# Performance work log

Hardware: AMD Instinct MI355X
Metric: run time of the kernel (lower is better)

Reference implementation:

```python
import jax, jax.numpy as jnp
import numpy as np

S, D, H, FF = 2048, 1024, 16, 4096
DH = D // H
EPS = 1e-5


def gelu(x):
    return 0.5 * x * (1 + jnp.tanh(jnp.sqrt(2 / jnp.pi) * (x + 0.044715 * jnp.power(x, 3))))


def layer_norm(x, w, b):
    mu = jnp.mean(x, axis=-1, keepdims=True)
    var = jnp.mean(jnp.square(x - mu), axis=-1, keepdims=True)
    return (x - mu) * jnp.power(var + EPS, -0.5) * w + b


def glorot(key, shape):
    fan_in, fan_out = shape[0], shape[1]
    lim = jnp.sqrt(6.0 / (fan_in + fan_out))
    return jax.random.uniform(key, shape, jnp.float32, -lim, lim)


def setup_inputs() -> dict:
    key = jax.random.key(0)
    ks = jax.random.split(key, 6)
    return {
        "x": jax.random.normal(ks[0], (S, D), jnp.float32),
        "W_qkv": glorot(ks[1], (D, 3 * D)),
        "W_o": glorot(ks[2], (D, D)),
        "W1": glorot(ks[3], (D, FF)),
        "b1": jnp.zeros((FF,), jnp.float32),
        "W2": glorot(ks[4], (FF, D)),
        "b2": jnp.zeros((D,), jnp.float32),
        "ln_att_w": jnp.ones((D,), jnp.float32),
        "ln_att_b": jnp.zeros((D,), jnp.float32),
        "ln_mlp_w": jnp.ones((D,), jnp.float32),
        "ln_mlp_b": jnp.zeros((D,), jnp.float32),
    }


def attention(x, W_qkv, W_o):
    qkv = (x @ W_qkv).reshape(S, 3, H, DH)
    q, k, v = qkv[:, 0], qkv[:, 1], qkv[:, 2]  # each [S, H, DH]
    # scores [H, S_q, S_k]
    scores = jnp.einsum("qhd,khd->hqk", q, k) / jnp.sqrt(jnp.float32(DH))
    causal = jnp.tril(jnp.ones((S, S), bool))
    scores = jnp.where(causal[None], scores, -jnp.inf)
    w = jax.nn.softmax(scores, axis=2)
    out = jnp.einsum("hqk,khd->qhd", w, v).reshape(S, D)
    return out @ W_o


def reference(x, W_qkv, W_o, W1, b1, W2, b2, ln_att_w, ln_att_b, ln_mlp_w, ln_mlp_b):
    x = x + attention(layer_norm(x, ln_att_w, ln_att_b), W_qkv, W_o)
    h = layer_norm(x, ln_mlp_w, ln_mlp_b)
    mlp_out = gelu(h @ W1 + b1) @ W2 + b2
    return x + mlp_out
```

## Files before the change

kernel.cpp:

```cpp
#include <hip/hip_runtime.h>
#include <math.h>

typedef __bf16 bf16;
typedef __bf16 bf16x4 __attribute__((ext_vector_type(4)));
typedef __bf16 bf16x8 __attribute__((ext_vector_type(8)));
typedef float f32x4 __attribute__((ext_vector_type(4)));
typedef unsigned short u16;
typedef unsigned short u16x8 __attribute__((ext_vector_type(8)));
typedef unsigned int u32;

__device__ __forceinline__ u16 f2bf(float f) {
  union { float f; u32 u; } v; v.f = f;
  u32 u = v.u;
  return (u16)((u + 0x7FFFu + ((u >> 16) & 1u)) >> 16);
}
__device__ __forceinline__ float bf2f(u16 u) {
  union { u32 u; float f; } v; v.u = (u32)u << 16;
  return v.f;
}

__device__ __forceinline__ f32x4 mfma16(bf16x8 a, bf16x8 b, f32x4 c) {
  return __builtin_amdgcn_mfma_f32_16x16x32_bf16(a, b, c, 0, 0, 0);
}

__device__ __forceinline__ size_t pk_addr(int r, int c, int C) {
  return ((size_t)(r >> 4) * (C >> 5) + (c >> 5)) * 512 +
         ((c >> 3) & 3) * 128 + (r & 15) * 8 + (c & 7);
}

__device__ __forceinline__ void wconv_body(const float* __restrict__ W,
                                           u16* __restrict__ Wt, int K, int N,
                                           int bx, int by) {
  __shared__ float tile[64][65];
  const int k0 = by * 64, n0 = bx * 64;
  const int t = threadIdx.x;
  const int tr = t >> 4;
  const int tc = (t & 15) * 4;
#pragma unroll
  for (int it = 0; it < 4; it++) {
    const int r = tr + it * 16;
    const float4 v = *(const float4*)(W + (size_t)(k0 + r) * N + n0 + tc);
    tile[r][tc] = v.x; tile[r][tc + 1] = v.y; tile[r][tc + 2] = v.z; tile[r][tc + 3] = v.w;
  }
  __syncthreads();
#pragma unroll
  for (int it = 0; it < 4; it++) {
    const int rn = tr + it * 16;
    const int n = n0 + rn;
    const int k = k0 + tc;
    ushort4 o;
    o.x = f2bf(tile[tc][rn]);
    o.y = f2bf(tile[tc + 1][rn]);
    o.z = f2bf(tile[tc + 2][rn]);
    o.w = f2bf(tile[tc + 3][rn]);
    *(ushort4*)(Wt + pk_addr(n, k, K)) = o;
  }
}

__global__ __launch_bounds__(256)
void wconv_all(const float* __restrict__ Wqkv, const float* __restrict__ Wo,
               const float* __restrict__ W1, const float* __restrict__ W2,
               u16* __restrict__ Wqkv_t, u16* __restrict__ Wo_t,
               u16* __restrict__ W1_t, u16* __restrict__ W2_t) {
  const int id = blockIdx.x;
  if (id < 768)       { wconv_body(Wqkv, Wqkv_t, 1024, 3072, id % 48, id / 48); }
  else if (id < 1024) { const int j = id - 768;  wconv_body(Wo, Wo_t, 1024, 1024, j % 16, j / 16); }
  else if (id < 2048) { const int j = id - 1024; wconv_body(W1, W1_t, 1024, 4096, j % 64, j / 64); }
  else                { const int j = id - 2048; wconv_body(W2, W2_t, 4096, 1024, j % 16, j / 16); }
}

__global__ __launch_bounds__(256)
void ln_bf16(const float* __restrict__ x, const float* __restrict__ w,
             const float* __restrict__ b, u16* __restrict__ out) {
  const int row = blockIdx.x;
  const int t = threadIdx.x;
  const float4 v = *(const float4*)(x + (size_t)row * 1024 + t * 4);
  float s = v.x + v.y + v.z + v.w;
  float s2 = v.x * v.x + v.y * v.y + v.z * v.z + v.w * v.w;
#pragma unroll
  for (int m = 1; m < 64; m <<= 1) {
    s += __shfl_xor(s, m);
    s2 += __shfl_xor(s2, m);
  }
  __shared__ float red[8];
  if ((t & 63) == 0) { red[t >> 6] = s; red[4 + (t >> 6)] = s2; }
  __syncthreads();
  s = red[0] + red[1] + red[2] + red[3];
  s2 = red[4] + red[5] + red[6] + red[7];
  const float mu = s * (1.f / 1024.f);
  const float var = fmaxf(s2 * (1.f / 1024.f) - mu * mu, 0.f);
  const float rstd = rsqrtf(var + 1e-5f);
  const float* wp = w + t * 4;
  const float* bp = b + t * 4;
  ushort4 o;
  o.x = f2bf((v.x - mu) * rstd * wp[0] + bp[0]);
  o.y = f2bf((v.y - mu) * rstd * wp[1] + bp[1]);
  o.z = f2bf((v.z - mu) * rstd * wp[2] + bp[2]);
  o.w = f2bf((v.w - mu) * rstd * wp[3] + bp[3]);
  *(ushort4*)(out + pk_addr(row, t * 4, 1024)) = o;
}

__global__ __launch_bounds__(256)
void reduce_ln(const float* __restrict__ x, const u16* __restrict__ pb,
               const float* __restrict__ w, const float* __restrict__ b,
               float* __restrict__ x2, u16* __restrict__ h2) {
  const int row = blockIdx.x;
  const int t = threadIdx.x;
  const size_t base = (size_t)row * 1024 + t * 4;
  float4 v = *(const float4*)(x + base);
#pragma unroll
  for (int z = 0; z < 4; z++) {
    const ushort4 p = *(const ushort4*)(pb + (size_t)z * 2097152 + base);
    v.x += bf2f(p.x); v.y += bf2f(p.y); v.z += bf2f(p.z); v.w += bf2f(p.w);
  }
  *(float4*)(x2 + base) = v;
  float s = v.x + v.y + v.z + v.w;
  float s2 = v.x * v.x + v.y * v.y + v.z * v.z + v.w * v.w;
#pragma unroll
  for (int m = 1; m < 64; m <<= 1) {
    s += __shfl_xor(s, m);
    s2 += __shfl_xor(s2, m);
  }
  __shared__ float red[8];
  if ((t & 63) == 0) { red[t >> 6] = s; red[4 + (t >> 6)] = s2; }
  __syncthreads();
  s = red[0] + red[1] + red[2] + red[3];
  s2 = red[4] + red[5] + red[6] + red[7];
  const float mu = s * (1.f / 1024.f);
  const float var = fmaxf(s2 * (1.f / 1024.f) - mu * mu, 0.f);
  const float rstd = rsqrtf(var + 1e-5f);
  const float* wp = w + t * 4;
  const float* bp = b + t * 4;
  ushort4 o;
  o.x = f2bf((v.x - mu) * rstd * wp[0] + bp[0]);
  o.y = f2bf((v.y - mu) * rstd * wp[1] + bp[1]);
  o.z = f2bf((v.z - mu) * rstd * wp[2] + bp[2]);
  o.w = f2bf((v.w - mu) * rstd * wp[3] + bp[3]);
  *(ushort4*)(h2 + pk_addr(row, t * 4, 1024)) = o;
}

__global__ __launch_bounds__(256)
void reduce_out(const float* __restrict__ x2, const float* __restrict__ bias,
                const u16* __restrict__ pb, float* __restrict__ out) {
  const size_t base = ((size_t)blockIdx.x * 256 + threadIdx.x) * 4;
  const int col = (int)(base & 1023);
  float4 v = *(const float4*)(x2 + base);
  const float4 bb = *(const float4*)(bias + col);
  v.x += bb.x; v.y += bb.y; v.z += bb.z; v.w += bb.w;
#pragma unroll
  for (int z = 0; z < 4; z++) {
    const ushort4 p = *(const ushort4*)(pb + (size_t)z * 2097152 + base);
    v.x += bf2f(p.x); v.y += bf2f(p.y); v.z += bf2f(p.z); v.w += bf2f(p.w);
  }
  *(float4*)(out + base) = v;
}

template <int EPI, int KS>
__global__ __launch_bounds__(256)
void gemm_pk(const u16* __restrict__ Ap, const u16* __restrict__ Bp,
             int M, int N, int K,
             const float* __restrict__ bias, u16* __restrict__ pb,
             u16* __restrict__ outB,
             u16* __restrict__ qo, u16* __restrict__ ko, u16* __restrict__ vo) {
  const int t = threadIdx.x;
  const int l = t & 63;
  const int w = t >> 6;
  const int WR = (w >> 1) * 64, WC = (w & 1) * 64;
  const int l15 = l & 15, lg = l >> 4;

  const int nx = gridDim.x;
  const u32 bid = blockIdx.y * nx + blockIdx.x;
  const int nxc = nx >> 3;
  const u32 r = bid >> 3;
  const int bx = (bid & 7) * nxc + (int)(r % (u32)nxc);
  const int by = (int)(r / (u32)nxc);

  const int m0 = by * 128, n0 = bx * 128;
  const int KT = K >> 5;
  const int nt = (K / KS) >> 5;
  const int t0 = blockIdx.z * nt;

  const u16* aB = Ap + ((size_t)((m0 + WR) >> 4) * KT + t0) * 512 + l * 8;
  const u16* bB = Bp + ((size_t)((n0 + WC) >> 4) * KT + t0) * 512 + l * 8;

  f32x4 acc[4][4] = {};
  bf16x8 a0[4], b0[4], a1[4], b1[4];

  auto LD = [&](bf16x8 (&af)[4], bf16x8 (&bf_)[4], int ti) {
#pragma unroll
    for (int i = 0; i < 4; i++)
      af[i] = *(const bf16x8*)(aB + ((size_t)i * KT + ti) * 512);
#pragma unroll
    for (int j = 0; j < 4; j++)
      bf_[j] = *(const bf16x8*)(bB + ((size_t)j * KT + ti) * 512);
  };
  auto FMA = [&](bf16x8 (&af)[4], bf16x8 (&bf_)[4]) {
    __builtin_amdgcn_s_setprio(1);
#pragma unroll
    for (int i = 0; i < 4; i++)
#pragma unroll
      for (int j = 0; j < 4; j++)
        acc[i][j] = mfma16(af[i], bf_[j], acc[i][j]);
    __builtin_amdgcn_s_setprio(0);
  };

  LD(a0, b0, 0);
  for (int ti = 0; ti < nt; ti += 2) {
    LD(a1, b1, (ti + 1 < nt) ? ti + 1 : ti);
    FMA(a0, b0);
    LD(a0, b0, (ti + 2 < nt) ? ti + 2 : ti);
    FMA(a1, b1);
  }

  const int mr0 = m0 + WR + lg * 4;
  const int nc0 = n0 + WC + l15;
#pragma unroll
  for (int i = 0; i < 4; i++) {
    const int mr = mr0 + i * 16;
#pragma unroll
    for (int j = 0; j < 4; j++) {
      const int nc = nc0 + j * 16;
      if (EPI == 0) {
        const int sel = nc >> 10;
        const int d = nc & 1023;
        const int h = d >> 6, dl = d & 63;
        const int kt2 = mr >> 5;
        if (sel == 2) {
          const int lgp = (mr >> 3) & 3, el0 = mr & 7;
          const int nb = dl >> 4, l15p = dl & 15;
          u16* dst = vo + (size_t)(h * 64 + kt2) * 2048 + nb * 512 +
                     (lgp * 16 + l15p) * 8 + el0;
          ushort4 o;
          o.x = f2bf(acc[i][j][0]); o.y = f2bf(acc[i][j][1]);
          o.z = f2bf(acc[i][j][2]); o.w = f2bf(acc[i][j][3]);
          *(ushort4*)dst = o;
        } else {
          const int f = (mr >> 4) & 1, l15p0 = mr & 15;
          const int kk = dl >> 5, lgp = (dl >> 3) & 3, el = dl & 7;
          u16* dst = (sel == 0 ? qo : ko) + (size_t)(h * 64 + kt2) * 2048 +
                     f * 1024 + kk * 512 + (lgp * 16 + l15p0) * 8 + el;
#pragma unroll
          for (int e = 0; e < 4; e++)
            dst[e * 8] = f2bf(acc[i][j][e]);
        }
      } else if (EPI == 2) {
        const float bb = bias[nc];
#pragma unroll
        for (int e = 0; e < 4; e++) {
          const float v = acc[i][j][e] + bb;
          const float g = 0.5f * v * (1.0f + tanhf(0.7978845608028654f * (v + 0.044715f * v * v * v)));
          outB[pk_addr(mr + e, nc, 4096)] = f2bf(g);
        }
      } else {
        u16* po = pb + (size_t)blockIdx.z * M * N;
#pragma unroll
        for (int e = 0; e < 4; e++)
          po[(size_t)(mr + e) * N + nc] = f2bf(acc[i][j][e]);
      }
    }
  }
}

__device__ __forceinline__ void attn_load(
    bf16x8 (&kf)[2][2], bf16x8 (&vf)[4],
    const u16* __restrict__ Kp, const u16* __restrict__ Vp,
    int hkt, int l) {
#pragma unroll
  for (int f = 0; f < 2; f++)
#pragma unroll
    for (int kk = 0; kk < 2; kk++)
      kf[kk][f] = *(const bf16x8*)(Kp + hkt + f * 1024 + kk * 512 + l * 8);
#pragma unroll
  for (int nb = 0; nb < 4; nb++)
    vf[nb] = *(const bf16x8*)(Vp + hkt + nb * 512 + l * 8);
}

__device__ __forceinline__ void attn_tile(
    const bf16x8 (&kf)[2][2], const bf16x8 (&vf)[4], const bf16x8 (&qf)[2][2],
    f32x4 (&accO)[2][4], float (&lsum)[2], u16* myP,
    int k0, bool diag, int qb, int l15, int lg) {
  f32x4 sv[2][2] = {};
  __builtin_amdgcn_s_setprio(1);
#pragma unroll
  for (int g = 0; g < 2; g++)
#pragma unroll
    for (int f = 0; f < 2; f++)
#pragma unroll
      for (int kk = 0; kk < 2; kk++)
        sv[g][f] = mfma16(kf[kk][f], qf[g][kk], sv[g][f]);
  __builtin_amdgcn_s_setprio(0);
#pragma unroll
  for (int g = 0; g < 2; g++) {
#pragma unroll
    for (int f = 0; f < 2; f++) {
      bf16x4 pk;
      float ps = 0.f;
#pragma unroll
      for (int e = 0; e < 4; e++) {
        float p = exp2f(sv[g][f][e] * 0.1803368801f);
        if (diag && (k0 + f * 16 + lg * 4 + e > qb + g * 16 + l15)) p = 0.f;
        ps += p;
        pk[e] = (bf16)p;
      }
      lsum[g] += ps;
      *(bf16x4*)(myP + g * 640 + l15 * 40 + f * 16 + lg * 4) = pk;
    }
  }
  const bf16x8 pf0 = *(const bf16x8*)(myP + l15 * 40 + lg * 8);
  const bf16x8 pf1 = *(const bf16x8*)(myP + 640 + l15 * 40 + lg * 8);
  __builtin_amdgcn_s_setprio(1);
#pragma unroll
  for (int nb = 0; nb < 4; nb++) {
    accO[0][nb] = mfma16(pf0, vf[nb], accO[0][nb]);
    accO[1][nb] = mfma16(pf1, vf[nb], accO[1][nb]);
  }
  __builtin_amdgcn_s_setprio(0);
}

__global__ __launch_bounds__(256)
void attn_fwd(const u16* __restrict__ Qp, const u16* __restrict__ Kp,
              const u16* __restrict__ Vp, u16* __restrict__ Ob) {
  __shared__ __attribute__((aligned(16))) char smem[33280];
  float* sO = (float*)smem;
  float* sL = (float*)(smem + 32768);
  u16* lP = (u16*)smem;

  const int t = threadIdx.x;
  const int l = t & 63, w = t >> 6;
  const int l15 = l & 15, lg = l >> 4;
  const u32 bid = blockIdx.x;
  const u32 vb = (bid & 7) * 128 + (bid >> 3);
  const int h = (int)(vb >> 6);
  const int qt = 63 - (int)(vb & 63);
  const int qb = qt * 32;

  u16* myPA = lP + w * 1280;
  u16* myPB = lP + 5120 + w * 1280;

  bf16x8 qf[2][2];
#pragma unroll
  for (int g = 0; g < 2; g++)
#pragma unroll
    for (int kk = 0; kk < 2; kk++)
      qf[g][kk] = *(const bf16x8*)(Qp + (size_t)(h * 64 + qt) * 2048 +
                                   g * 1024 + kk * 512 + l * 8);

  f32x4 accO[2][4] = {};
  float lsum[2] = {0.f, 0.f};

  if (w <= qt) {
    const int hb = h * 64;
    bf16x8 kfA[2][2], vfA[4], kfB[2][2], vfB[4];
    attn_load(kfA, vfA, Kp, Vp, (hb + w) * 2048, l);
    int kt = w;
    while (true) {
      const int ktB = kt + 4;
      const bool hasB = (ktB <= qt);
      attn_load(kfB, vfB, Kp, Vp, (hb + (hasB ? ktB : kt)) * 2048, l);
      attn_tile(kfA, vfA, qf, accO, lsum, myPA, kt * 32, kt == qt, qb, l15, lg);
      if (!hasB) break;
      const int ktA = kt + 8;
      const bool hasA = (ktA <= qt);
      attn_load(kfA, vfA, Kp, Vp, (hb + (hasA ? ktA : ktB)) * 2048, l);
      attn_tile(kfB, vfB, qf, accO, lsum, myPB, ktB * 32, ktB == qt, qb, l15, lg);
      if (!hasA) break;
      kt = ktA;
    }
  }

  float lsr[2];
#pragma unroll
  for (int g = 0; g < 2; g++) {
    float v = lsum[g];
    v += __shfl_xor(v, 16);
    v += __shfl_xor(v, 32);
    lsr[g] = v;
  }

  __syncthreads();
#pragma unroll
  for (int g = 0; g < 2; g++) {
#pragma unroll
    for (int nb = 0; nb < 4; nb++)
#pragma unroll
      for (int e = 0; e < 4; e++)
        sO[w * 2048 + (g * 16 + lg * 4 + e) * 64 + nb * 16 + l15] = accO[g][nb][e];
    if (lg == 0) sL[w * 32 + g * 16 + l15] = lsr[g];
  }
  __syncthreads();

  const int base = t * 8;
  const int row = base >> 6;
  const int col = base & 63;
  f32x4 a0 = {}, a1 = {};
  float ls = 0.f;
#pragma unroll
  for (int ww = 0; ww < 4; ww++) {
    a0 += *(const f32x4*)&sO[ww * 2048 + base];
    a1 += *(const f32x4*)&sO[ww * 2048 + base + 4];
    ls += sL[ww * 32 + row];
  }
  const float rinv = 1.0f / ls;
  u16x8 o;
#pragma unroll
  for (int j = 0; j < 4; j++) {
    o[j] = f2bf(a0[j] * rinv);
    o[4 + j] = f2bf(a1[j] * rinv);
  }
  const int grow = qb + row;
  const int gcol = h * 64 + col;
  *(u16x8*)(Ob + pk_addr(grow, gcol, 1024)) = o;
}

extern "C" void kernel_launch(void* const* d_in, const int* in_sizes, int n_in,
                              void* d_out, int out_size, void* d_ws, size_t ws_size,
                              hipStream_t stream) {
  const float* x     = (const float*)d_in[0];
  const float* W_qkv = (const float*)d_in[1];
  const float* W_o   = (const float*)d_in[2];
  const float* W1    = (const float*)d_in[3];
  const float* b1    = (const float*)d_in[4];
  const float* W2    = (const float*)d_in[5];
  const float* b2    = (const float*)d_in[6];
  const float* ln_aw = (const float*)d_in[7];
  const float* ln_ab = (const float*)d_in[8];
  const float* ln_mw = (const float*)d_in[9];
  const float* ln_mb = (const float*)d_in[10];

  char* ws = (char*)d_ws;
  u16* Wqkv_t = (u16*)(ws);
  u16* Wo_t   = (u16*)(ws + 6291456);
  u16* W1_t   = (u16*)(ws + 8388608);
  u16* W2_t   = (u16*)(ws + 16777216);
  u16* h1     = (u16*)(ws + 25165824);
  u16* h2     = h1;
  u16* Qp     = (u16*)(ws + 29360128);
  u16* Kp     = (u16*)(ws + 33554432);
  u16* Vp     = (u16*)(ws + 37748736);
  u16* attnb  = (u16*)(ws + 41943040);
  u16* ffb    = (u16*)(ws + 29360128);
  u16* pb     = (u16*)(ws + 46137344);
  float* x2   = (float*)(ws + 62914560);
  (void)ws_size; (void)in_sizes; (void)n_in; (void)out_size;

  wconv_all<<<3072, 256, 0, stream>>>(W_qkv, W_o, W1, W2, Wqkv_t, Wo_t, W1_t, W2_t);

  ln_bf16<<<2048, 256, 0, stream>>>(x, ln_aw, ln_ab, h1);

  gemm_pk<0, 1><<<dim3(24, 16), 256, 0, stream>>>(
      h1, Wqkv_t, 2048, 3072, 1024, nullptr, nullptr, nullptr, Qp, Kp, Vp);

  attn_fwd<<<1024, 256, 0, stream>>>(Qp, Kp, Vp, attnb);

  gemm_pk<4, 4><<<dim3(8, 16, 4), 256, 0, stream>>>(
      attnb, Wo_t, 2048, 1024, 1024, nullptr, pb, nullptr, nullptr, nullptr, nullptr);

  reduce_ln<<<2048, 256, 0, stream>>>(x, pb, ln_mw, ln_mb, x2, h2);

  gemm_pk<2, 1><<<dim3(32, 16), 256, 0, stream>>>(
      h2, W1_t, 2048, 4096, 1024, b1, nullptr, ffb, nullptr, nullptr, nullptr);

  gemm_pk<4, 4><<<dim3(8, 16, 4), 256, 0, stream>>>(
      ffb, W2_t, 2048, 1024, 4096, nullptr, pb, nullptr, nullptr, nullptr, nullptr);

  reduce_out<<<2048, 256, 0, stream>>>(x2, b2, pb, (float*)d_out);
}
```

Before: 151.4 us.

## Merge weight conversion with first layernorm and deepen GEMM register prefetch

Folds the first layernorm into the weight-conversion kernel as extra blocks, saving one launch and letting the two independent jobs overlap. The GEMM's register double buffer becomes a four-stage rotation that keeps loads two k-tiles ahead of the MFMAs, to hide more global-load latency. It also adds a launch-bounds occupancy hint of 2, which together with the extra fragment registers may force spills or cut occupancy. The loop now steps by 4 tiles and always preloads tile 1, which assumes nt is a multiple of 4, as it is for these shapes.

New measurement: 154.2 us. Within noise of the previous version (+1.9%).

```diff
diff --git a/kernel.cpp b/kernel.cpp
--- a/kernel.cpp
+++ b/kernel.cpp
@@ -57,22 +57,10 @@
   }
 }
 
-__global__ __launch_bounds__(256)
-void wconv_all(const float* __restrict__ Wqkv, const float* __restrict__ Wo,
-               const float* __restrict__ W1, const float* __restrict__ W2,
-               u16* __restrict__ Wqkv_t, u16* __restrict__ Wo_t,
-               u16* __restrict__ W1_t, u16* __restrict__ W2_t) {
-  const int id = blockIdx.x;
-  if (id < 768)       { wconv_body(Wqkv, Wqkv_t, 1024, 3072, id % 48, id / 48); }
-  else if (id < 1024) { const int j = id - 768;  wconv_body(Wo, Wo_t, 1024, 1024, j % 16, j / 16); }
-  else if (id < 2048) { const int j = id - 1024; wconv_body(W1, W1_t, 1024, 4096, j % 64, j / 64); }
-  else                { const int j = id - 2048; wconv_body(W2, W2_t, 4096, 1024, j % 16, j / 16); }
-}
-
-__global__ __launch_bounds__(256)
-void ln_bf16(const float* __restrict__ x, const float* __restrict__ w,
-             const float* __restrict__ b, u16* __restrict__ out) {
-  const int row = blockIdx.x;
+__device__ __forceinline__ void ln_body(const float* __restrict__ x,
+                                        const float* __restrict__ w,
+                                        const float* __restrict__ b,
+                                        u16* __restrict__ out, int row) {
   const int t = threadIdx.x;
   const float4 v = *(const float4*)(x + (size_t)row * 1024 + t * 4);
   float s = v.x + v.y + v.z + v.w;
@@ -101,6 +89,22 @@
 }
 
 __global__ __launch_bounds__(256)
+void prep_all(const float* __restrict__ Wqkv, const float* __restrict__ Wo,
+              const float* __restrict__ W1, const float* __restrict__ W2,
+              const float* __restrict__ x, const float* __restrict__ ln_aw,
+              const float* __restrict__ ln_ab,
+              u16* __restrict__ Wqkv_t, u16* __restrict__ Wo_t,
+              u16* __restrict__ W1_t, u16* __restrict__ W2_t,
+              u16* __restrict__ h1) {
+  const int id = blockIdx.x;
+  if (id < 768)       { wconv_body(Wqkv, Wqkv_t, 1024, 3072, id % 48, id / 48); }
+  else if (id < 1024) { const int j = id - 768;  wconv_body(Wo, Wo_t, 1024, 1024, j % 16, j / 16); }
+  else if (id < 2048) { const int j = id - 1024; wconv_body(W1, W1_t, 1024, 4096, j % 64, j / 64); }
+  else if (id < 3072) { const int j = id - 2048; wconv_body(W2, W2_t, 4096, 1024, j % 16, j / 16); }
+  else                { ln_body(x, ln_aw, ln_ab, h1, id - 3072); }
+}
+
+__global__ __launch_bounds__(256)
 void reduce_ln(const float* __restrict__ x, const u16* __restrict__ pb,
                const float* __restrict__ w, const float* __restrict__ b,
                float* __restrict__ x2, u16* __restrict__ h2) {
@@ -156,7 +160,7 @@
 }
 
 template <int EPI, int KS>
-__global__ __launch_bounds__(256)
+__global__ __launch_bounds__(256, 2)
 void gemm_pk(const u16* __restrict__ Ap, const u16* __restrict__ Bp,
              int M, int N, int K,
              const float* __restrict__ bias, u16* __restrict__ pb,
@@ -184,7 +188,7 @@
   const u16* bB = Bp + ((size_t)((n0 + WC) >> 4) * KT + t0) * 512 + l * 8;
 
   f32x4 acc[4][4] = {};
-  bf16x8 a0[4], b0[4], a1[4], b1[4];
+  bf16x8 a0[4], b0[4], a1[4], b1[4], a2[4], b2[4], a3[4], b3[4];
 
   auto LD = [&](bf16x8 (&af)[4], bf16x8 (&bf_)[4], int ti) {
 #pragma unroll
@@ -205,11 +209,12 @@
   };
 
   LD(a0, b0, 0);
-  for (int ti = 0; ti < nt; ti += 2) {
-    LD(a1, b1, (ti + 1 < nt) ? ti + 1 : ti);
-    FMA(a0, b0);
-    LD(a0, b0, (ti + 2 < nt) ? ti + 2 : ti);
-    FMA(a1, b1);
+  LD(a1, b1, 1);
+  for (int ti = 0; ti < nt; ti += 4) {
+    LD(a2, b2, (ti + 2 < nt) ? ti + 2 : ti);  FMA(a0, b0);
+    LD(a3, b3, (ti + 3 < nt) ? ti + 3 : ti);  FMA(a1, b1);
+    LD(a0, b0, (ti + 4 < nt) ? ti + 4 : ti);  FMA(a2, b2);
+    LD(a1, b1, (ti + 5 < nt) ? ti + 5 : ti);  FMA(a3, b3);
   }
 
   const int mr0 = m0 + WR + lg * 4;
@@ -443,9 +448,8 @@
   float* x2   = (float*)(ws + 62914560);
   (void)ws_size; (void)in_sizes; (void)n_in; (void)out_size;
 
-  wconv_all<<<3072, 256, 0, stream>>>(W_qkv, W_o, W1, W2, Wqkv_t, Wo_t, W1_t, W2_t);
-
-  ln_bf16<<<2048, 256, 0, stream>>>(x, ln_aw, ln_ab, h1);
+  prep_all<<<5120, 256, 0, stream>>>(W_qkv, W_o, W1, W2, x, ln_aw, ln_ab,
+                                     Wqkv_t, Wo_t, W1_t, W2_t, h1);
 
   gemm_pk<0, 1><<<dim3(24, 16), 256, 0, stream>>>(
       h1, Wqkv_t, 2048, 3072, 1024, nullptr, nullptr, nullptr, Qp, Kp, Vp);
```
